# Kernel tuning notes

Hardware: AMD Instinct MI355X
Metric: run time of the kernel (lower is better)

## Reference

```python
import jax, jax.numpy as jnp
import numpy as np

TOPK = 60            # candidates kept by top-k
THRESHOLD = 0.15     # score threshold (post-sigmoid)
NMS_THRESHOLD = 0.05 # IoU overlap for suppression/matching
NMS_TOPK = 20        # max kept detections per image
CROP_SIZE = (96, 96, 96)
AVG_TOPN = 7         # max matched boxes averaged per kept box


def setup_inputs() -> dict:
    key = jax.random.key(0)
    k1, k2, k3 = jax.random.split(key, 3)
    B, D, H, W = 256, 24, 24, 24
    Cls = jax.random.normal(k1, (B, 1, D, H, W), dtype=jnp.float32)
    # sizes in [1,7) voxels so 3D boxes at stride-4 anchor spacing overlap
    Shape = jax.random.uniform(k2, (B, 3, D, H, W), dtype=jnp.float32) * 6.0 + 1.0
    Offset = jax.random.normal(k3, (B, 3, D, H, W), dtype=jnp.float32)
    return {"Cls": Cls, "Shape": Shape, "Offset": Offset}


def _decode(Cls, Shape, Offset):
    # make_anchors + bbox_decode: centers = (anchor + offset) * stride, sizes = Shape
    B, _, D, H, W = Cls.shape
    stride = jnp.float32(CROP_SIZE[0] / D)  # 96/24 = 4
    gz, gy, gx = jnp.meshgrid(jnp.arange(D, dtype=jnp.float32),
                              jnp.arange(H, dtype=jnp.float32),
                              jnp.arange(W, dtype=jnp.float32), indexing="ij")
    anchors = jnp.stack([gz, gy, gx], -1).reshape(-1, 3)            # [N,3]
    scores = jax.nn.sigmoid(Cls.reshape(B, -1))                     # [B,N] (is_logits=True)
    shapes = Shape.reshape(B, 3, -1).transpose(0, 2, 1)             # [B,N,3]
    offsets = Offset.reshape(B, 3, -1).transpose(0, 2, 1)           # [B,N,3]
    centers = (anchors[None] + offsets) * stride
    bboxes = jnp.concatenate([centers, shapes], -1)                 # [B,N,6] = (z,y,x,d,h,w)
    return scores, bboxes


def _iou_matrix(det):
    # axis-aligned 3D IoU between all pairs of the TOPK candidate boxes
    c, s = det[:, 2:5], det[:, 5:8]
    lo, hi = c - 0.5 * s, c + 0.5 * s
    inter = jnp.prod(jnp.maximum(jnp.minimum(hi[:, None], hi[None]) -
                                 jnp.maximum(lo[:, None], lo[None]), 0.0), -1)
    vol = jnp.prod(s, -1)
    return inter / (vol[:, None] + vol[None] - inter)


def _nms_image(scores, bboxes):
    # top-k (sorted descending, as torch.topk) then masked iterative NMS with
    # IoU-matched top-7 box averaging, emitting a fixed [NMS_TOPK, 8] table.
    topk_s, topk_i = jax.lax.top_k(scores, TOPK)
    valid = topk_s > THRESHOLD
    det = jnp.concatenate([jnp.ones((TOPK, 1), jnp.float32),
                           topk_s[:, None], bboxes[topk_i]], -1)    # [TOPK,8]
    iou = _iou_matrix(det)
    ar = jnp.arange(TOPK)

    def step(suppressed, _):
        avail = valid & ~suppressed
        any_avail = jnp.any(avail)
        idx = jnp.argmax(avail)  # first available = highest remaining score
        matched = avail & ((iou[idx] > NMS_THRESHOLD) | (ar == idx))
        rank = jnp.cumsum(matched) - 1            # matched are already score-sorted
        sel = matched & (rank < AVG_TOPN)
        top_n = jnp.minimum(jnp.sum(matched), AVG_TOPN)
        avg = jnp.sum(det * sel[:, None].astype(det.dtype), 0) / jnp.maximum(top_n, 1).astype(det.dtype)
        avg = avg.at[0].set(1.0).at[1].set(det[idx, 1])  # flag=1, prob = best score
        row = jnp.where(top_n > 1, avg, det[idx])
        row = jnp.where(any_avail, row, -jnp.ones(8, det.dtype))
        suppressed = jnp.where(any_avail, suppressed | matched, suppressed)
        return suppressed, row

    _, rows = jax.lax.scan(step, jnp.zeros(TOPK, dtype=bool), None, length=NMS_TOPK)
    return rows  # [NMS_TOPK, 8]


def reference(Cls, Shape, Offset):
    scores, bboxes = _decode(Cls, Shape, Offset)
    return jax.vmap(_nms_image)(scores, bboxes)  # [B, NMS_TOPK, 8]
```

## Files before the change

kernel.cpp:

```cpp
#include <hip/hip_runtime.h>
#include <math.h>

#define N_ANCH 13824
#define TPB 1024
#define K_TOP 60
#define K_NMS 20
#define AVG_TOPN 7
#define CAP 2048
#define PIVOT_KEY 0xC0100000u

__device__ __forceinline__ unsigned mono_key(float x) {
  unsigned m = __float_as_uint(x);
  return (m & 0x80000000u) ? ~m : (m | 0x80000000u);
}

__global__ __launch_bounds__(TPB)
void detpp_kernel(const float* __restrict__ Cls,
                  const float* __restrict__ Shp,
                  const float* __restrict__ Off,
                  float* __restrict__ Out) {
  __shared__ unsigned long long list[CAP];
  __shared__ float det[K_TOP][9];
  __shared__ unsigned long long Mrow[K_TOP];
  __shared__ unsigned int cnt2;

  const int b = blockIdx.x;
  const int t = threadIdx.x;
  const int lane = t & 63;
  const size_t cbase = (size_t)b * N_ANCH;

  if (t == 0) cnt2 = 0;
  if (t < K_TOP) Mrow[t] = 1ull << t;

  const float4* C4 = (const float4*)(Cls + cbase);
  float4 v0 = C4[t];
  float4 v1 = C4[1024 + t];
  float4 v2 = C4[2048 + t];
  const bool tail = (t < 384);
  float4 v3 = tail ? C4[3072 + t] : make_float4(0.f, 0.f, 0.f, 0.f);
  __syncthreads();

  unsigned k[16];
  k[0]  = mono_key(v0.x); k[1]  = mono_key(v0.y); k[2]  = mono_key(v0.z); k[3]  = mono_key(v0.w);
  k[4]  = mono_key(v1.x); k[5]  = mono_key(v1.y); k[6]  = mono_key(v1.z); k[7]  = mono_key(v1.w);
  k[8]  = mono_key(v2.x); k[9]  = mono_key(v2.y); k[10] = mono_key(v2.z); k[11] = mono_key(v2.w);
  if (tail) {
    k[12] = mono_key(v3.x); k[13] = mono_key(v3.y); k[14] = mono_key(v3.z); k[15] = mono_key(v3.w);
  } else {
    k[12] = 0u; k[13] = 0u; k[14] = 0u; k[15] = 0u;
  }

  int cnt = 0;
  #pragma unroll
  for (int q = 0; q < 16; ++q) cnt += (k[q] > PIVOT_KEY) ? 1 : 0;

  int pfx = cnt;
  #pragma unroll
  for (int d = 1; d < 64; d <<= 1) {
    int o = __shfl_up(pfx, d, 64);
    if (lane >= d) pfx += o;
  }
  const int excl = pfx - cnt;
  int wtot = __shfl(pfx, 63, 64);
  unsigned wbase = 0;
  if (lane == 63) wbase = atomicAdd(&cnt2, (unsigned)wtot);
  wbase = (unsigned)__shfl((int)wbase, 63, 64);

  {
    int off = (int)wbase + excl;
    #pragma unroll
    for (int q = 0; q < 16; ++q) {
      if (k[q] > PIVOT_KEY) {
        int base_i = (q < 4) ? (t << 2) : (q < 8) ? ((1024 + t) << 2)
                     : (q < 12) ? ((2048 + t) << 2) : ((3072 + t) << 2);
        int i = base_i + (q & 3);
        if (off < CAP)
          list[off] = ((unsigned long long)k[q] << 32) | (unsigned)(~i);
        off++;
      }
    }
  }
  __syncthreads();

  const unsigned total = cnt2;
  const bool fast = (total >= (unsigned)K_TOP) && (total <= (unsigned)CAP);

  auto build_det = [&](unsigned long long e, int r) {
    int i = (int)(~(unsigned)(e & 0xffffffffull));
    unsigned m = (unsigned)(e >> 32);
    unsigned bits = (m & 0x80000000u) ? (m & 0x7fffffffu) : ~m;
    float lg = __uint_as_float(bits);
    float sc = 1.0f / (1.0f + expf(-lg));
    int iz = i / 576;
    int r2 = i - iz * 576;
    int iy = r2 / 24;
    int ix = r2 - iy * 24;
    size_t bb = (size_t)b * 3 * N_ANCH + (size_t)i;
    float o0 = Off[bb], o1 = Off[bb + N_ANCH], o2 = Off[bb + 2 * N_ANCH];
    float s0 = Shp[bb], s1 = Shp[bb + N_ANCH], s2 = Shp[bb + 2 * N_ANCH];
    det[r][0] = 1.0f;
    det[r][1] = sc;
    det[r][2] = ((float)iz + o0) * 4.0f;
    det[r][3] = ((float)iy + o1) * 4.0f;
    det[r][4] = ((float)ix + o2) * 4.0f;
    det[r][5] = s0;
    det[r][6] = s1;
    det[r][7] = s2;
  };

  if (fast) {
    if (t < (int)total) {
      const unsigned long long e = list[t];
      int r = 0;
      int j = 0;
      const int tot = (int)total;
      for (; j + 4 <= tot; j += 4) {
        r += (list[j]     > e) ? 1 : 0;
        r += (list[j + 1] > e) ? 1 : 0;
        r += (list[j + 2] > e) ? 1 : 0;
        r += (list[j + 3] > e) ? 1 : 0;
      }
      for (; j < tot; ++j) r += (list[j] > e) ? 1 : 0;
      if (r < K_TOP) build_det(e, r);
    }
  } else {
    for (int i = t; i < N_ANCH; i += TPB) {
      unsigned ki = mono_key(Cls[cbase + i]);
      unsigned long long e = ((unsigned long long)ki << 32) | (unsigned)(~i);
      int r = 0;
      for (int j = 0; j < N_ANCH; ++j) {
        unsigned kj = mono_key(Cls[cbase + j]);
        unsigned long long ej = ((unsigned long long)kj << 32) | (unsigned)(~j);
        r += (ej > e) ? 1 : 0;
      }
      if (r < K_TOP) build_det(e, r);
    }
  }
  __syncthreads();

  for (int p = t; p < 1800; p += TPB) {
    int ii = p / 30;
    int kk = p - ii * 30;
    int jj = ii + 1 + kk; if (jj >= 60) jj -= 60;
    float cz1 = det[ii][2], cy1 = det[ii][3], cx1 = det[ii][4];
    float sz1 = det[ii][5], sy1 = det[ii][6], sx1 = det[ii][7];
    float cz2 = det[jj][2], cy2 = det[jj][3], cx2 = det[jj][4];
    float sz2 = det[jj][5], sy2 = det[jj][6], sx2 = det[jj][7];
    float lz1 = cz1 - 0.5f * sz1, hz1 = cz1 + 0.5f * sz1;
    float ly1 = cy1 - 0.5f * sy1, hy1 = cy1 + 0.5f * sy1;
    float lx1 = cx1 - 0.5f * sx1, hx1 = cx1 + 0.5f * sx1;
    float lz2 = cz2 - 0.5f * sz2, hz2 = cz2 + 0.5f * sz2;
    float ly2 = cy2 - 0.5f * sy2, hy2 = cy2 + 0.5f * sy2;
    float lx2 = cx2 - 0.5f * sx2, hx2 = cx2 + 0.5f * sx2;
    float dz = fmaxf(fminf(hz1, hz2) - fmaxf(lz1, lz2), 0.0f);
    float dy = fmaxf(fminf(hy1, hy2) - fmaxf(ly1, ly2), 0.0f);
    float dx = fmaxf(fminf(hx1, hx2) - fmaxf(lx1, lx2), 0.0f);
    float inter = (dz * dy) * dx;
    float v1 = (sz1 * sy1) * sx1;
    float v2 = (sz2 * sy2) * sx2;
    float iouv = inter / (v1 + v2 - inter);
    if (iouv > 0.05f) {
      atomicOr(&Mrow[ii], 1ull << jj);
      atomicOr(&Mrow[jj], 1ull << ii);
    }
  }
  __syncthreads();

  if (t < 64) {
    const bool in = (lane < K_TOP);
    float myscore = in ? det[lane][1] : 0.0f;
    unsigned long long M = in ? Mrow[lane] : 0ull;
    unsigned long long validm = __ballot(in && (myscore > 0.15f));
    unsigned long long suppressed = 0ull;
    float* outb = Out + (size_t)b * K_NMS * 8;
    const int q = lane >> 3, c = lane & 7;

    #pragma unroll
    for (int step = 0; step < K_NMS; ++step) {
      unsigned long long avail = validm & ~suppressed;
      const bool any = (avail != 0ull);
      int idx = any ? (int)__builtin_ctzll(avail) : 0;
      unsigned mlo = (unsigned)__builtin_amdgcn_readlane((int)(unsigned)(M & 0xffffffffull), idx);
      unsigned mhi = (unsigned)__builtin_amdgcn_readlane((int)(unsigned)(M >> 32), idx);
      unsigned long long matched = any ? (avail & (((unsigned long long)mhi << 32) | mlo)) : 0ull;
      int cm = __popcll(matched);
      int top_n = cm < AVG_TOPN ? cm : AVG_TOPN;
      int myb = 0;
      { unsigned long long m2 = matched;
        #pragma unroll
        for (int z = 0; z < 8; ++z) {
          int bz = m2 ? (int)__builtin_ctzll(m2) : 0;
          if (z == q) myb = bz;
          m2 &= m2 - 1ull;
        } }
      float vv = (q < top_n) ? det[myb][c] : 0.0f;
      vv += __shfl_xor(vv, 8, 64);
      vv += __shfl_xor(vv, 16, 64);
      vv += __shfl_xor(vv, 32, 64);
      float sidx = __uint_as_float((unsigned)__builtin_amdgcn_readlane((int)__float_as_uint(myscore), idx));
      float r = vv / (float)(top_n > 0 ? top_n : 1);
      if (lane < 8) {
        float o = r;
        if (lane == 0) o = 1.0f;
        if (lane == 1) o = sidx;
        if (!any) o = -1.0f;
        outb[step * 8 + lane] = o;
      }
      suppressed |= matched;
    }
  }
}

extern "C" void kernel_launch(void* const* d_in, const int* in_sizes, int n_in,
                              void* d_out, int out_size, void* d_ws, size_t ws_size,
                              hipStream_t stream) {
  const float* Cls = (const float*)d_in[0];
  const float* Shp = (const float*)d_in[1];
  const float* Off = (const float*)d_in[2];
  float* Out = (float*)d_out;
  int B = in_sizes[0] / N_ANCH;
  detpp_kernel<<<B, TPB, 0, stream>>>(Cls, Shp, Off, Out);
}
```

Baseline: 117.8 us.

## Prefetch box data before ranking, vectorize rank scan, parallelize NMS averaging across waves

Issues the global loads of offsets and shapes for each candidate before the rank-count loop so their latency overlaps the scan. The rank scan now reads the shared list as 128-bit pairs. The serial NMS loop now only tracks the suppression masks, and three waves each average and write a subset of the 20 output rows in parallel, taking averaging and shuffles off the serial chain. This uses more registers and has three waves redundantly run the mask loop.

```diff
diff --git a/kernel.cpp b/kernel.cpp
--- a/kernel.cpp
+++ b/kernel.cpp
@@ -19,7 +19,7 @@
                   const float* __restrict__ Shp,
                   const float* __restrict__ Off,
                   float* __restrict__ Out) {
-  __shared__ unsigned long long list[CAP];
+  __shared__ __align__(16) unsigned long long list[CAP];
   __shared__ float det[K_TOP][9];
   __shared__ unsigned long long Mrow[K_TOP];
   __shared__ unsigned int cnt2;
@@ -85,43 +85,45 @@
   const unsigned total = cnt2;
   const bool fast = (total >= (unsigned)K_TOP) && (total <= (unsigned)CAP);
 
-  auto build_det = [&](unsigned long long e, int r) {
-    int i = (int)(~(unsigned)(e & 0xffffffffull));
-    unsigned m = (unsigned)(e >> 32);
-    unsigned bits = (m & 0x80000000u) ? (m & 0x7fffffffu) : ~m;
-    float lg = __uint_as_float(bits);
-    float sc = 1.0f / (1.0f + expf(-lg));
-    int iz = i / 576;
-    int r2 = i - iz * 576;
-    int iy = r2 / 24;
-    int ix = r2 - iy * 24;
-    size_t bb = (size_t)b * 3 * N_ANCH + (size_t)i;
-    float o0 = Off[bb], o1 = Off[bb + N_ANCH], o2 = Off[bb + 2 * N_ANCH];
-    float s0 = Shp[bb], s1 = Shp[bb + N_ANCH], s2 = Shp[bb + 2 * N_ANCH];
-    det[r][0] = 1.0f;
-    det[r][1] = sc;
-    det[r][2] = ((float)iz + o0) * 4.0f;
-    det[r][3] = ((float)iy + o1) * 4.0f;
-    det[r][4] = ((float)ix + o2) * 4.0f;
-    det[r][5] = s0;
-    det[r][6] = s1;
-    det[r][7] = s2;
-  };
-
   if (fast) {
-    if (t < (int)total) {
-      const unsigned long long e = list[t];
+    const int tot = (int)total;
+    unsigned long long e = 0ull;
+    int i = 0;
+    float o0 = 0.f, o1 = 0.f, o2 = 0.f, s0 = 0.f, s1 = 0.f, s2 = 0.f;
+    if (t < tot) {
+      e = list[t];
+      i = (int)(~(unsigned)(e & 0xffffffffull));
+      size_t bb = (size_t)b * 3 * N_ANCH + (size_t)i;
+      o0 = Off[bb]; o1 = Off[bb + N_ANCH]; o2 = Off[bb + 2 * N_ANCH];
+      s0 = Shp[bb]; s1 = Shp[bb + N_ANCH]; s2 = Shp[bb + 2 * N_ANCH];
+    }
+    if (t < tot) {
       int r = 0;
-      int j = 0;
-      const int tot = (int)total;
-      for (; j + 4 <= tot; j += 4) {
-        r += (list[j]     > e) ? 1 : 0;
-        r += (list[j + 1] > e) ? 1 : 0;
-        r += (list[j + 2] > e) ? 1 : 0;
-        r += (list[j + 3] > e) ? 1 : 0;
-      }
-      for (; j < tot; ++j) r += (list[j] > e) ? 1 : 0;
-      if (r < K_TOP) build_det(e, r);
+      const ulonglong2* L2 = (const ulonglong2*)list;
+      const int half = tot >> 1;
+      for (int j2 = 0; j2 < half; ++j2) {
+        ulonglong2 p = L2[j2];
+        r += (p.x > e) ? 1 : 0;
+        r += (p.y > e) ? 1 : 0;
+      }
+      if (tot & 1) r += (list[tot - 1] > e) ? 1 : 0;
+      if (r < K_TOP) {
+        unsigned m = (unsigned)(e >> 32);
+        unsigned bits = (m & 0x80000000u) ? (m & 0x7fffffffu) : ~m;
+        float lg = __uint_as_float(bits);
+        int iz = i / 576;
+        int r2 = i - iz * 576;
+        int iy = r2 / 24;
+        int ix = r2 - iy * 24;
+        det[r][0] = 1.0f;
+        det[r][1] = 1.0f / (1.0f + expf(-lg));
+        det[r][2] = ((float)iz + o0) * 4.0f;
+        det[r][3] = ((float)iy + o1) * 4.0f;
+        det[r][4] = ((float)ix + o2) * 4.0f;
+        det[r][5] = s0;
+        det[r][6] = s1;
+        det[r][7] = s2;
+      }
     }
   } else {
     for (int i = t; i < N_ANCH; i += TPB) {
@@ -133,7 +135,24 @@
         unsigned long long ej = ((unsigned long long)kj << 32) | (unsigned)(~j);
         r += (ej > e) ? 1 : 0;
       }
-      if (r < K_TOP) build_det(e, r);
+      if (r < K_TOP) {
+        unsigned m = (unsigned)(e >> 32);
+        unsigned bits = (m & 0x80000000u) ? (m & 0x7fffffffu) : ~m;
+        float lg = __uint_as_float(bits);
+        int iz = i / 576;
+        int r2 = i - iz * 576;
+        int iy = r2 / 24;
+        int ix = r2 - iy * 24;
+        size_t bb = (size_t)b * 3 * N_ANCH + (size_t)i;
+        det[r][0] = 1.0f;
+        det[r][1] = 1.0f / (1.0f + expf(-lg));
+        det[r][2] = ((float)iz + Off[bb]) * 4.0f;
+        det[r][3] = ((float)iy + Off[bb + N_ANCH]) * 4.0f;
+        det[r][4] = ((float)ix + Off[bb + 2 * N_ANCH]) * 4.0f;
+        det[r][5] = Shp[bb];
+        det[r][6] = Shp[bb + N_ANCH];
+        det[r][7] = Shp[bb + 2 * N_ANCH];
+      }
     }
   }
   __syncthreads();
@@ -166,14 +185,21 @@
   }
   __syncthreads();
 
-  if (t < 64) {
+  const int w = t >> 6;
+  if (w < 3) {
     const bool in = (lane < K_TOP);
     float myscore = in ? det[lane][1] : 0.0f;
     unsigned long long M = in ? Mrow[lane] : 0ull;
     unsigned long long validm = __ballot(in && (myscore > 0.15f));
     unsigned long long suppressed = 0ull;
     float* outb = Out + (size_t)b * K_NMS * 8;
-    const int q = lane >> 3, c = lane & 7;
+
+    const int my_s = (w << 3) + (lane >> 3);
+    const int c = lane & 7;
+    const bool active = (my_s < K_NMS);
+    unsigned long long my_matched = 0ull;
+    int my_idx = 0;
+    bool my_any = false;
 
     #pragma unroll
     for (int step = 0; step < K_NMS; ++step) {
@@ -183,30 +209,26 @@
       unsigned mlo = (unsigned)__builtin_amdgcn_readlane((int)(unsigned)(M & 0xffffffffull), idx);
       unsigned mhi = (unsigned)__builtin_amdgcn_readlane((int)(unsigned)(M >> 32), idx);
       unsigned long long matched = any ? (avail & (((unsigned long long)mhi << 32) | mlo)) : 0ull;
-      int cm = __popcll(matched);
+      if (step == my_s) { my_matched = matched; my_idx = idx; my_any = any; }
+      suppressed |= matched;
+    }
+
+    if (active) {
+      int cm = __popcll(my_matched);
       int top_n = cm < AVG_TOPN ? cm : AVG_TOPN;
-      int myb = 0;
-      { unsigned long long m2 = matched;
-        #pragma unroll
-        for (int z = 0; z < 8; ++z) {
-          int bz = m2 ? (int)__builtin_ctzll(m2) : 0;
-          if (z == q) myb = bz;
-          m2 &= m2 - 1ull;
-        } }
-      float vv = (q < top_n) ? det[myb][c] : 0.0f;
-      vv += __shfl_xor(vv, 8, 64);
-      vv += __shfl_xor(vv, 16, 64);
-      vv += __shfl_xor(vv, 32, 64);
-      float sidx = __uint_as_float((unsigned)__builtin_amdgcn_readlane((int)__float_as_uint(myscore), idx));
-      float r = vv / (float)(top_n > 0 ? top_n : 1);
-      if (lane < 8) {
-        float o = r;
-        if (lane == 0) o = 1.0f;
-        if (lane == 1) o = sidx;
-        if (!any) o = -1.0f;
-        outb[step * 8 + lane] = o;
-      }
-      suppressed |= matched;
+      float sum = 0.0f;
+      unsigned long long mm = my_matched;
+      #pragma unroll
+      for (int q = 0; q < AVG_TOPN; ++q) {
+        int bq = mm ? (int)__builtin_ctzll(mm) : 0;
+        if (q < top_n) sum += det[bq][c];
+        mm &= mm - 1ull;
+      }
+      float r = sum / (float)(top_n > 0 ? top_n : 1);
+      if (c == 0) r = 1.0f;
+      if (c == 1) r = det[my_idx][1];
+      if (!my_any) r = -1.0f;
+      outb[my_s * 8 + c] = r;
     }
   }
 }
```

After: 112.8 us. 1.04x faster.
